# Performance work log

Hardware: AMD Instinct MI355X
Metric: run time of the kernel (lower is better)

The kernel has to match this reference:

```python
import jax, jax.numpy as jnp
import numpy as np
from jax import lax

B, T, IN, H, L, OUT = 24, 8192, 55, 110, 4, 23


def _indrnn_layer(x, w, u, bias):
    # x: [B, T, D_in]; w: [H, D_in]; u, bias: [H]
    # pre-activation input contribution can be batched as one GEMM
    pre = jnp.einsum('btd,hd->bth', x, w) + bias  # [B, T, H]

    def step(h, p):  # h: [B, H], p: [B, H]
        h = jax.nn.relu(p + u * h)
        return h, h

    h0 = jnp.zeros((x.shape[0], w.shape[0]), dtype=x.dtype)
    _, hs = lax.scan(step, h0, jnp.swapaxes(pre, 0, 1))  # hs: [T, B, H]
    return jnp.swapaxes(hs, 0, 1)  # [B, T, H]


def setup_inputs() -> dict:
    key = jax.random.key(0)
    ks = jax.random.split(key, 9)
    s = 0.1  # weight scale to keep the long relu recurrence bounded
    x = jax.random.normal(ks[0], (B, T, IN), dtype=jnp.float32)
    w_ih0 = jax.random.normal(ks[1], (H, IN), dtype=jnp.float32) * s
    w_ih1 = jax.random.normal(ks[2], (H, H), dtype=jnp.float32) * s
    w_ih2 = jax.random.normal(ks[3], (H, H), dtype=jnp.float32) * s
    w_ih3 = jax.random.normal(ks[4], (H, H), dtype=jnp.float32) * s
    u = jax.random.uniform(ks[5], (L, H), dtype=jnp.float32) * 0.9  # |u| < 1
    b = jax.random.normal(ks[6], (L, H), dtype=jnp.float32) * s
    w_out = jax.random.normal(ks[7], (OUT, H), dtype=jnp.float32) * s
    b_out = jax.random.normal(ks[8], (OUT,), dtype=jnp.float32) * s
    return {'x': x, 'w_ih0': w_ih0, 'w_ih1': w_ih1, 'w_ih2': w_ih2,
            'w_ih3': w_ih3, 'u': u, 'b': b, 'w_out': w_out, 'b_out': b_out}


def reference(x, w_ih0, w_ih1, w_ih2, w_ih3, u, b, w_out, b_out):
    h = x
    for i, w in enumerate([w_ih0, w_ih1, w_ih2, w_ih3]):
        h = _indrnn_layer(h, w, u[i], b[i])  # [B, T, H]
    last = h[:, -1, :]                       # [B, H]
    logits = last @ w_out.T + b_out          # [B, OUT]
    return jax.nn.log_softmax(logits, axis=1)
```

## Files before the change

### kernel.cpp

```cpp
#include <hip/hip_runtime.h>
#include <math.h>

#define B_SZ 24
#define T_SZ 8192
#define IN_SZ 55
#define H_SZ 110
#define OUT_SZ 23

constexpr int CHUNK = 512;
constexpr int WARM  = 256;
constexpr int PF    = 32;
constexpr int TAIL  = 768;

typedef __attribute__((ext_vector_type(8))) _Float16 f16x8;
typedef __attribute__((ext_vector_type(4))) float    f32x4;

__device__ __forceinline__ unsigned int pack2h(float x, float y) {
    _Float16 a = (_Float16)x, b = (_Float16)y;
    return (unsigned int)__builtin_bit_cast(unsigned short, a) |
           ((unsigned int)__builtin_bit_cast(unsigned short, b) << 16);
}

__global__ __launch_bounds__(256)
void conv_x_kernel(const float* __restrict__ x, unsigned int* __restrict__ xh)
{
    const size_t total = (size_t)B_SZ * T_SZ * 32;
    for (size_t i = (size_t)blockIdx.x * 256 + threadIdx.x; i < total;
         i += (size_t)gridDim.x * 256) {
        const size_t r = i >> 5; const int cp = (int)(i & 31);
        const int c0 = 2 * cp, c1 = 2 * cp + 1;
        const float v0 = (c0 < IN_SZ) ? x[r * IN_SZ + c0] : 0.f;
        const float v1 = (c1 < IN_SZ) ? x[r * IN_SZ + c1] : 0.f;
        xh[i] = pack2h(v0, v1);
    }
}

template<int KREAL, int LDA, int RPB>
__global__ __launch_bounds__(256)
void mfma_gemm(const _Float16* __restrict__ A, const float* __restrict__ W,
               const float* __restrict__ bias, float* __restrict__ P,
               int mt_per_wave, int t_offset)
{
    constexpr int KS = LDA / 32;
    const int tid  = threadIdx.x;
    const int wave = tid >> 6;
    const int lane = tid & 63;
    const int g    = wave & 1;
    const int mp   = wave >> 1;
    const int lrow = lane & 15;
    const int lgrp = lane >> 4;

    f16x8 bf[4][KS];
    float bb[4];
    #pragma unroll
    for (int nt = 0; nt < 4; nt++) {
        const int j = g * 64 + nt * 16 + lrow;
        bb[nt] = (j < H_SZ) ? bias[j] : 0.f;
        #pragma unroll
        for (int ks = 0; ks < KS; ks++) {
            f16x8 v;
            #pragma unroll
            for (int i = 0; i < 8; i++) {
                const int k = ks * 32 + lgrp * 8 + i;
                const float w = (j < H_SZ && k < KREAL) ? W[(size_t)j * KREAL + k] : 0.f;
                v[i] = (_Float16)w;
            }
            bf[nt][ks] = v;
        }
    }

    const int m_base = blockIdx.x * (mt_per_wave * 32);
    for (int it = 0; it < mt_per_wave; it++) {
        const int m0 = m_base + (it * 2 + mp) * 16;
        const int m  = m0 + lrow;
        const int arow = (m / RPB) * T_SZ + t_offset + (m % RPB);
        const _Float16* ap = A + (size_t)arow * LDA + lgrp * 8;

        f16x8 a[KS];
        #pragma unroll
        for (int ks = 0; ks < KS; ks++) a[ks] = *(const f16x8*)(ap + ks * 32);

        f32x4 acc[4];
        #pragma unroll
        for (int nt = 0; nt < 4; nt++) acc[nt] = (f32x4){bb[nt], bb[nt], bb[nt], bb[nt]};

        #pragma unroll
        for (int ks = 0; ks < KS; ks++)
            #pragma unroll
            for (int nt = 0; nt < 4; nt++)
                acc[nt] = __builtin_amdgcn_mfma_f32_16x16x32_f16(a[ks], bf[nt][ks], acc[nt], 0, 0, 0);

        float* Pout = P + (size_t)m0 * H_SZ;
        #pragma unroll
        for (int nt = 0; nt < 4; nt++) {
            const int col = g * 64 + nt * 16 + lrow;
            if (col < H_SZ) {
                #pragma unroll
                for (int r = 0; r < 4; r++)
                    Pout[(size_t)(lgrp * 4 + r) * H_SZ + col] = acc[nt][r];
            }
        }
    }
}

__global__ __launch_bounds__(64)
void scan_kernel(const float* __restrict__ Pre, const float* __restrict__ u_,
                 unsigned int* __restrict__ Hh, int Tin, int chunk, int out_off)
{
    const int j = threadIdx.x;
    const bool valid = (j < 55);
    const int jj = valid ? j : 0;
    const int b    = blockIdx.y;
    const int t0   = blockIdx.x * chunk;
    const int tw   = (t0 > WARM) ? (t0 - WARM) : 0;
    const int tend = t0 + chunk;

    float2 u = make_float2(0.f, 0.f);
    if (valid) u = *reinterpret_cast<const float2*>(u_ + 2 * j);
    const float2* p = reinterpret_cast<const float2*>(Pre + (size_t)b * Tin * H_SZ) + jj;
    const size_t orow0 = (size_t)b * T_SZ + out_off;

    float2 h = make_float2(0.f, 0.f);
    float2 Abuf[PF], Bbuf[PF];

    #pragma unroll
    for (int i = 0; i < PF; i++) Abuf[i] = p[(size_t)(tw + i) * 55];

    for (int tb = tw; tb < tend; tb += 2 * PF) {
        #pragma unroll
        for (int i = 0; i < PF; i++) Bbuf[i] = p[(size_t)(tb + PF + i) * 55];
        #pragma unroll
        for (int i = 0; i < PF; i++) {
            h.x = fmaxf(fmaf(u.x, h.x, Abuf[i].x), 0.f);
            h.y = fmaxf(fmaf(u.y, h.y, Abuf[i].y), 0.f);
            const int t = tb + i;
            if (t >= t0)
                Hh[(orow0 + t) * 64 + j] = valid ? pack2h(h.x, h.y) : 0u;
        }
        if (tb + 2 * PF < tend) {
            #pragma unroll
            for (int i = 0; i < PF; i++) Abuf[i] = p[(size_t)(tb + 2 * PF + i) * 55];
        }
        #pragma unroll
        for (int i = 0; i < PF; i++) {
            h.x = fmaxf(fmaf(u.x, h.x, Bbuf[i].x), 0.f);
            h.y = fmaxf(fmaf(u.y, h.y, Bbuf[i].y), 0.f);
            const int t = tb + PF + i;
            if (t >= t0)
                Hh[(orow0 + t) * 64 + j] = valid ? pack2h(h.x, h.y) : 0u;
        }
    }
}

__global__ __launch_bounds__(256)
void head_kernel(const _Float16* __restrict__ Hh, const float* __restrict__ Wo,
                 const float* __restrict__ bo, float* __restrict__ out)
{
    __shared__ float last[B_SZ][112];
    __shared__ float wsh[OUT_SZ][112];
    __shared__ float logits[B_SZ][32];
    const int tid = threadIdx.x;

    for (int idx = tid; idx < B_SZ * H_SZ; idx += 256) {
        const int b = idx / H_SZ, jj = idx - b * H_SZ;
        last[b][jj] = (float)Hh[((size_t)b * T_SZ + T_SZ - 1) * 128 + jj];
    }
    for (int idx = tid; idx < OUT_SZ * H_SZ; idx += 256) {
        const int oo = idx / H_SZ, jj = idx - oo * H_SZ;
        wsh[oo][jj] = Wo[idx];
    }
    __syncthreads();

    for (int idx = tid; idx < B_SZ * OUT_SZ; idx += 256) {
        const int b = idx / OUT_SZ, o = idx - b * OUT_SZ;
        float s = bo[o];
        for (int k = 0; k < H_SZ; k++) s = fmaf(last[b][k], wsh[o][k], s);
        logits[b][o] = s;
    }
    __syncthreads();

    if (tid < B_SZ) {
        const int b = tid;
        float m = -1e30f;
        for (int o = 0; o < OUT_SZ; o++) m = fmaxf(m, logits[b][o]);
        float sum = 0.f;
        for (int o = 0; o < OUT_SZ; o++) sum += expf(logits[b][o] - m);
        const float lse = m + logf(sum);
        for (int o = 0; o < OUT_SZ; o++) out[b * OUT_SZ + o] = logits[b][o] - lse;
    }
}

extern "C" void kernel_launch(void* const* d_in, const int* in_sizes, int n_in,
                              void* d_out, int out_size, void* d_ws, size_t ws_size,
                              hipStream_t stream)
{
    const float* x  = (const float*)d_in[0];
    const float* w0 = (const float*)d_in[1];
    const float* w1 = (const float*)d_in[2];
    const float* w2 = (const float*)d_in[3];
    const float* w3 = (const float*)d_in[4];
    const float* u  = (const float*)d_in[5];
    const float* bi = (const float*)d_in[6];
    const float* wo = (const float*)d_in[7];
    const float* bo = (const float*)d_in[8];
    float* out = (float*)d_out;

    const size_t M = (size_t)B_SZ * T_SZ;
    float* P = (float*)d_ws;
    _Float16* A = (_Float16*)((char*)d_ws + M * H_SZ * 4);
    unsigned int* Au = (unsigned int*)A;

    conv_x_kernel<<<4096, 256, 0, stream>>>(x, Au);
    mfma_gemm<IN_SZ, 64, T_SZ><<<384, 256, 0, stream>>>(A, w0, bi, P, 16, 0);
    scan_kernel<<<dim3(T_SZ / CHUNK, B_SZ), 64, 0, stream>>>(P, u, Au, T_SZ, CHUNK, 0);
    mfma_gemm<H_SZ, 128, T_SZ><<<384, 256, 0, stream>>>(A, w1, bi + H_SZ, P, 16, 0);
    scan_kernel<<<dim3(T_SZ / CHUNK, B_SZ), 64, 0, stream>>>(P, u + H_SZ, Au, T_SZ, CHUNK, 0);
    mfma_gemm<H_SZ, 128, T_SZ><<<384, 256, 0, stream>>>(A, w2, bi + 2 * H_SZ, P, 16, 0);
    scan_kernel<<<dim3(T_SZ / CHUNK, B_SZ), 64, 0, stream>>>(P, u + 2 * H_SZ, Au, T_SZ, CHUNK, 0);
    mfma_gemm<H_SZ, 128, TAIL><<<72, 256, 0, stream>>>(A, w3, bi + 3 * H_SZ, P, 8, T_SZ - TAIL);
    scan_kernel<<<dim3(1, B_SZ), 64, 0, stream>>>(P, u + 3 * H_SZ, Au, TAIL, TAIL, T_SZ - TAIL);
    head_kernel<<<1, 256, 0, stream>>>(A, wo, bo, out);
}
```

Before: 411.2 us.

## Store GEMM pre-activations as packed fp16 and double-buffer A loads

The GEMM now writes pre-activations as packed half2 words in a 64-word padded row instead of fp32 rows of 110. It pairs lanes with a shuffle to form each word, which halves the intermediate traffic between the GEMM and scan kernels. The scan kernel loads and unpacks these half2 words. The GEMM also double-buffers its A-fragment loads and launches twice as many blocks with half the tiles each, and the scan warmup window shrinks from 256 to 128 steps. The risks are extra rounding in the pre-activations and a less converged recurrence state at chunk boundaries.

```diff
diff --git a/kernel.cpp b/kernel.cpp
--- a/kernel.cpp
+++ b/kernel.cpp
@@ -8,7 +8,7 @@
 #define OUT_SZ 23
 
 constexpr int CHUNK = 512;
-constexpr int WARM  = 256;
+constexpr int WARM  = 128;
 constexpr int PF    = 32;
 constexpr int TAIL  = 768;
 
@@ -19,6 +19,11 @@
     _Float16 a = (_Float16)x, b = (_Float16)y;
     return (unsigned int)__builtin_bit_cast(unsigned short, a) |
            ((unsigned int)__builtin_bit_cast(unsigned short, b) << 16);
+}
+__device__ __forceinline__ float2 unpack2h(unsigned int w) {
+    const _Float16 lo = __builtin_bit_cast(_Float16, (unsigned short)(w & 0xffffu));
+    const _Float16 hi = __builtin_bit_cast(_Float16, (unsigned short)(w >> 16));
+    return make_float2((float)lo, (float)hi);
 }
 
 __global__ __launch_bounds__(256)
@@ -38,7 +43,7 @@
 template<int KREAL, int LDA, int RPB>
 __global__ __launch_bounds__(256)
 void mfma_gemm(const _Float16* __restrict__ A, const float* __restrict__ W,
-               const float* __restrict__ bias, float* __restrict__ P,
+               const float* __restrict__ bias, unsigned int* __restrict__ P,
                int mt_per_wave, int t_offset)
 {
     constexpr int KS = LDA / 32;
@@ -70,41 +75,50 @@
     }
 
     const int m_base = blockIdx.x * (mt_per_wave * 32);
-    for (int it = 0; it < mt_per_wave; it++) {
+
+    auto aload = [&](f16x8 (&a)[KS], int it) {
         const int m0 = m_base + (it * 2 + mp) * 16;
         const int m  = m0 + lrow;
         const int arow = (m / RPB) * T_SZ + t_offset + (m % RPB);
         const _Float16* ap = A + (size_t)arow * LDA + lgrp * 8;
-
-        f16x8 a[KS];
         #pragma unroll
         for (int ks = 0; ks < KS; ks++) a[ks] = *(const f16x8*)(ap + ks * 32);
-
+    };
+    auto compute_store = [&](f16x8 (&a)[KS], int it) {
+        const int m0 = m_base + (it * 2 + mp) * 16;
         f32x4 acc[4];
         #pragma unroll
         for (int nt = 0; nt < 4; nt++) acc[nt] = (f32x4){bb[nt], bb[nt], bb[nt], bb[nt]};
-
         #pragma unroll
         for (int ks = 0; ks < KS; ks++)
             #pragma unroll
             for (int nt = 0; nt < 4; nt++)
                 acc[nt] = __builtin_amdgcn_mfma_f32_16x16x32_f16(a[ks], bf[nt][ks], acc[nt], 0, 0, 0);
-
-        float* Pout = P + (size_t)m0 * H_SZ;
         #pragma unroll
         for (int nt = 0; nt < 4; nt++) {
-            const int col = g * 64 + nt * 16 + lrow;
-            if (col < H_SZ) {
-                #pragma unroll
-                for (int r = 0; r < 4; r++)
-                    Pout[(size_t)(lgrp * 4 + r) * H_SZ + col] = acc[nt][r];
+            #pragma unroll
+            for (int r = 0; r < 4; r++) {
+                const float other = __shfl_xor(acc[nt][r], 1);
+                if ((lane & 1) == 0) {
+                    const int c = g * 32 + nt * 8 + (lrow >> 1);
+                    P[(size_t)(m0 + lgrp * 4 + r) * 64 + c] = pack2h(acc[nt][r], other);
+                }
             }
         }
+    };
+
+    f16x8 a0[KS], a1[KS];
+    aload(a0, 0);
+    for (int it = 0; it < mt_per_wave; it += 2) {
+        aload(a1, it + 1);
+        compute_store(a0, it);
+        if (it + 2 < mt_per_wave) aload(a0, it + 2);
+        compute_store(a1, it + 1);
     }
 }
 
 __global__ __launch_bounds__(64)
-void scan_kernel(const float* __restrict__ Pre, const float* __restrict__ u_,
+void scan_kernel(const unsigned int* __restrict__ Pre, const float* __restrict__ u_,
                  unsigned int* __restrict__ Hh, int Tin, int chunk, int out_off)
 {
     const int j = threadIdx.x;
@@ -117,34 +131,36 @@
 
     float2 u = make_float2(0.f, 0.f);
     if (valid) u = *reinterpret_cast<const float2*>(u_ + 2 * j);
-    const float2* p = reinterpret_cast<const float2*>(Pre + (size_t)b * Tin * H_SZ) + jj;
+    const unsigned int* p = Pre + (size_t)b * Tin * 64 + jj;
     const size_t orow0 = (size_t)b * T_SZ + out_off;
 
     float2 h = make_float2(0.f, 0.f);
-    float2 Abuf[PF], Bbuf[PF];
+    unsigned int Abuf[PF], Bbuf[PF];
 
     #pragma unroll
-    for (int i = 0; i < PF; i++) Abuf[i] = p[(size_t)(tw + i) * 55];
+    for (int i = 0; i < PF; i++) Abuf[i] = p[(size_t)(tw + i) * 64];
 
     for (int tb = tw; tb < tend; tb += 2 * PF) {
         #pragma unroll
-        for (int i = 0; i < PF; i++) Bbuf[i] = p[(size_t)(tb + PF + i) * 55];
+        for (int i = 0; i < PF; i++) Bbuf[i] = p[(size_t)(tb + PF + i) * 64];
         #pragma unroll
         for (int i = 0; i < PF; i++) {
-            h.x = fmaxf(fmaf(u.x, h.x, Abuf[i].x), 0.f);
-            h.y = fmaxf(fmaf(u.y, h.y, Abuf[i].y), 0.f);
+            const float2 pv = unpack2h(Abuf[i]);
+            h.x = fmaxf(fmaf(u.x, h.x, pv.x), 0.f);
+            h.y = fmaxf(fmaf(u.y, h.y, pv.y), 0.f);
             const int t = tb + i;
             if (t >= t0)
                 Hh[(orow0 + t) * 64 + j] = valid ? pack2h(h.x, h.y) : 0u;
         }
         if (tb + 2 * PF < tend) {
             #pragma unroll
-            for (int i = 0; i < PF; i++) Abuf[i] = p[(size_t)(tb + 2 * PF + i) * 55];
+            for (int i = 0; i < PF; i++) Abuf[i] = p[(size_t)(tb + 2 * PF + i) * 64];
         }
         #pragma unroll
         for (int i = 0; i < PF; i++) {
-            h.x = fmaxf(fmaf(u.x, h.x, Bbuf[i].x), 0.f);
-            h.y = fmaxf(fmaf(u.y, h.y, Bbuf[i].y), 0.f);
+            const float2 pv = unpack2h(Bbuf[i]);
+            h.x = fmaxf(fmaf(u.x, h.x, pv.x), 0.f);
+            h.y = fmaxf(fmaf(u.y, h.y, pv.y), 0.f);
             const int t = tb + PF + i;
             if (t >= t0)
                 Hh[(orow0 + t) * 64 + j] = valid ? pack2h(h.x, h.y) : 0u;
@@ -206,16 +222,16 @@
     float* out = (float*)d_out;
 
     const size_t M = (size_t)B_SZ * T_SZ;
-    float* P = (float*)d_ws;
-    _Float16* A = (_Float16*)((char*)d_ws + M * H_SZ * 4);
+    unsigned int* P = (unsigned int*)d_ws;
+    _Float16* A = (_Float16*)((char*)d_ws + M * 64 * 4);
     unsigned int* Au = (unsigned int*)A;
 
     conv_x_kernel<<<4096, 256, 0, stream>>>(x, Au);
-    mfma_gemm<IN_SZ, 64, T_SZ><<<384, 256, 0, stream>>>(A, w0, bi, P, 16, 0);
+    mfma_gemm<IN_SZ, 64, T_SZ><<<768, 256, 0, stream>>>(A, w0, bi, P, 8, 0);
     scan_kernel<<<dim3(T_SZ / CHUNK, B_SZ), 64, 0, stream>>>(P, u, Au, T_SZ, CHUNK, 0);
-    mfma_gemm<H_SZ, 128, T_SZ><<<384, 256, 0, stream>>>(A, w1, bi + H_SZ, P, 16, 0);
+    mfma_gemm<H_SZ, 128, T_SZ><<<768, 256, 0, stream>>>(A, w1, bi + H_SZ, P, 8, 0);
     scan_kernel<<<dim3(T_SZ / CHUNK, B_SZ), 64, 0, stream>>>(P, u + H_SZ, Au, T_SZ, CHUNK, 0);
-    mfma_gemm<H_SZ, 128, T_SZ><<<384, 256, 0, stream>>>(A, w2, bi + 2 * H_SZ, P, 16, 0);
+    mfma_gemm<H_SZ, 128, T_SZ><<<768, 256, 0, stream>>>(A, w2, bi + 2 * H_SZ, P, 8, 0);
     scan_kernel<<<dim3(T_SZ / CHUNK, B_SZ), 64, 0, stream>>>(P, u + 2 * H_SZ, Au, T_SZ, CHUNK, 0);
     mfma_gemm<H_SZ, 128, TAIL><<<72, 256, 0, stream>>>(A, w3, bi + 3 * H_SZ, P, 8, T_SZ - TAIL);
     scan_kernel<<<dim3(1, B_SZ), 64, 0, stream>>>(P, u + 3 * H_SZ, Au, TAIL, TAIL, T_SZ - TAIL);
```

After: 387.9 us. 5.7% less time.
